# Kernel optimization log

Measured on AMD Instinct MI355X. Metric: run time of the kernel, lower is better.

The kernel has to match this reference:

```python
import jax, jax.numpy as jnp
import numpy as np


def _gcn_conv(x, src, dst, W, b, num_nodes, deg_inv_sqrt):
    # PyG GCNConv: h = x @ W, then normalized scatter-add over edges (incl. self loops), + bias
    h = x @ W  # [N, d_out]
    norm = deg_inv_sqrt[src] * deg_inv_sqrt[dst]  # [E']
    msg = h[src] * norm[:, None]  # gather + scale, [E', d_out]
    out = jax.ops.segment_sum(msg, dst, num_segments=num_nodes)  # scatter-add to targets
    return out + b


def reference(x, edge_index, W1, b1, W2, b2, num_nodes):
    src0, dst0 = edge_index[0], edge_index[1]
    loop = jnp.arange(num_nodes, dtype=edge_index.dtype)
    # add self loops (PyG default add_self_loops=True)
    src = jnp.concatenate([src0, loop])
    dst = jnp.concatenate([dst0, loop])
    # symmetric normalization D^{-1/2} (A+I) D^{-1/2}, degree from self-looped graph
    deg = jax.ops.segment_sum(jnp.ones_like(src, dtype=x.dtype), dst, num_segments=num_nodes)
    deg_inv_sqrt = jnp.where(deg > 0, jax.lax.rsqrt(jnp.maximum(deg, 1)), 0.0).astype(x.dtype)

    z = jax.nn.relu(_gcn_conv(x, src, dst, W1, b1, num_nodes, deg_inv_sqrt))
    z = jax.nn.relu(_gcn_conv(z, src, dst, W2, b2, num_nodes, deg_inv_sqrt))
    return z


def setup_inputs() -> dict:
    key = jax.random.key(0)
    k1, k2, k3, k4 = jax.random.split(key, 4)
    N, E, D, H = 50000, 1600000, 128, 128
    x = jax.random.normal(k1, (N, D), dtype=jnp.float32)
    edge_index = jax.random.randint(k2, (2, E), 0, N, dtype=jnp.int64)
    s = 1.0 / np.sqrt(D)
    W1 = jax.random.normal(k3, (D, H), dtype=jnp.float32) * s
    W2 = jax.random.normal(k4, (H, H), dtype=jnp.float32) * s
    return {
        "x": x,
        "edge_index": edge_index,
        "W1": W1,
        "b1": jnp.zeros((H,), jnp.float32),
        "W2": W2,
        "b2": jnp.zeros((H,), jnp.float32),
        "num_nodes": N,
    }
```

## Files before the change

### kernel.cpp

```cpp
#include <hip/hip_runtime.h>

#define FD 128
#define BSH 7
#define BPAD 16
#define CH 4096
#define CHT 16

typedef __attribute__((ext_vector_type(8))) short bf16x8;
typedef __attribute__((ext_vector_type(4))) float f32x4;

__device__ inline unsigned bfr(float f) {
    unsigned u = __float_as_uint(f);
    return (u + 0x7FFF + ((u >> 16) & 1)) >> 16;
}
__device__ inline float uplo(unsigned p) { return __uint_as_float(p << 16); }
__device__ inline float uphi(unsigned p) { return __uint_as_float(p & 0xFFFF0000u); }


__global__ __launch_bounds__(256) void hist_kernel(
        const int* __restrict__ dst, int* __restrict__ bhist, int E, int K) {
    __shared__ int lh[512];
    for (int i = threadIdx.x; i < K; i += 256) lh[i] = 0;
    __syncthreads();
    for (int e = blockIdx.x * 256 + threadIdx.x; e < E; e += gridDim.x * 256)
        atomicAdd(&lh[dst[e] >> BSH], 1);
    __syncthreads();
    for (int i = threadIdx.x; i < K; i += 256)
        if (lh[i]) atomicAdd(&bhist[i], lh[i]);
}

__global__ __launch_bounds__(512) void bscan_kernel(
        const int* __restrict__ bhist, int* __restrict__ bbase, int* __restrict__ bcur,
        int* __restrict__ rp, int K, int E, int N) {
    __shared__ int sm[512];
    int t = threadIdx.x;
    int v = (t < K) ? bhist[t] : 0;
    sm[t] = v;
    __syncthreads();
    for (int off = 1; off < 512; off <<= 1) {
        int add = (t >= off) ? sm[t - off] : 0;
        __syncthreads();
        sm[t] += add;
        __syncthreads();
    }
    if (t < K) { bbase[t] = sm[t] - v; bcur[t * BPAD] = sm[t] - v; }
    if (t == 0) { bbase[K] = E; rp[N] = E; }
}

__global__ __launch_bounds__(256) void partition_kernel(
        const int* __restrict__ src, const int* __restrict__ dst,
        int* __restrict__ bcur, int* __restrict__ pairs, int E) {
    __shared__ int   lcnt[512];
    __shared__ int   lstart[512];
    __shared__ int   ldelta[512];
    __shared__ int   sm[256];
    __shared__ int   staged[CH];
    __shared__ short binof[CH];
    int t = threadIdx.x;
    int base = blockIdx.x * CH;
    int n = min(CH, E - base);

    lcnt[t] = 0; lcnt[t + 256] = 0;
    __syncthreads();

    int pk[CHT]; int bn[CHT];
    #pragma unroll
    for (int j = 0; j < CHT; ++j) {
        int i = t + j * 256;
        bn[j] = -1;
        if (i < n) {
            int d = dst[base + i];
            int s = src[base + i];
            bn[j] = d >> BSH;
            pk[j] = ((d & ((1 << BSH) - 1)) << 17) | s;
            atomicAdd(&lcnt[bn[j]], 1);
        }
    }
    __syncthreads();

    int c0 = lcnt[2 * t], c1 = lcnt[2 * t + 1];
    int s2 = c0 + c1;
    sm[t] = s2;
    __syncthreads();
    for (int off = 1; off < 256; off <<= 1) {
        int add = (t >= off) ? sm[t - off] : 0;
        __syncthreads();
        sm[t] += add;
        __syncthreads();
    }
    int ex = sm[t] - s2;
    lstart[2 * t] = ex;     lstart[2 * t + 1] = ex + c0;
    lcnt[2 * t]   = ex;     lcnt[2 * t + 1]   = ex + c0;
    __syncthreads();

    #pragma unroll
    for (int j = 0; j < CHT; ++j) {
        if (bn[j] >= 0) {
            int pos = atomicAdd(&lcnt[bn[j]], 1);
            staged[pos] = pk[j];
            binof[pos] = (short)bn[j];
        }
    }
    __syncthreads();

    #pragma unroll
    for (int k = 0; k < 2; ++k) {
        int b = 2 * t + k;
        int cnt = lcnt[b] - lstart[b];
        if (cnt > 0) {
            int g = atomicAdd(&bcur[b * BPAD], cnt);
            ldelta[b] = g - lstart[b];
        }
    }
    __syncthreads();

    for (int i = t; i < n; i += 256)
        pairs[ldelta[binof[i]] + i] = staged[i];
}

__global__ __launch_bounds__(256) void build_kernel(
        const int* __restrict__ pairs, const int* __restrict__ bbase,
        int* __restrict__ rp, float* __restrict__ dis, int* __restrict__ col, int N) {
    __shared__ int lcnt[1 << BSH];
    __shared__ int lsum[1 << BSH];
    __shared__ int lbase[1 << BSH];
    int b = blockIdx.x;
    int t = threadIdx.x;
    int nbase = b << BSH;
    int nn = min(1 << BSH, N - nbase);
    int beg = bbase[b], end = bbase[b + 1];
    if (t < 128) lcnt[t] = 0;
    __syncthreads();
    for (int e = beg + t; e < end; e += 256)
        atomicAdd(&lcnt[pairs[e] >> 17], 1);
    __syncthreads();
    if (t < 128) lsum[t] = lcnt[t];
    __syncthreads();
    for (int off = 1; off < 128; off <<= 1) {
        int add = (t < 128 && t >= off) ? lsum[t - off] : 0;
        __syncthreads();
        if (t < 128) lsum[t] += add;
        __syncthreads();
    }
    if (t < 128) {
        int excl = beg + lsum[t] - lcnt[t];
        lbase[t] = excl;
        if (t < nn) {
            rp[nbase + t] = excl;
            dis[nbase + t] = rsqrtf((float)(lcnt[t] + 1));
        }
    }
    __syncthreads();
    if (t < 128) lcnt[t] = lbase[t];
    __syncthreads();
    for (int e = beg + t; e < end; e += 256) {
        int p = pairs[e];
        int pos = atomicAdd(&lcnt[p >> 17], 1);
        col[pos] = p & 0x1FFFF;
    }
}


__global__ void cvt_kernel(const float4* __restrict__ in, uint2* __restrict__ outp, int n4) {
    int i = blockIdx.x * blockDim.x + threadIdx.x;
    if (i < n4) {
        float4 v = in[i];
        uint2 o;
        o.x = bfr(v.x) | (bfr(v.y) << 16);
        o.y = bfr(v.z) | (bfr(v.w) << 16);
        outp[i] = o;
    }
}

__global__ void wt_kernel(const float* __restrict__ W, unsigned short* __restrict__ WT) {
    int k = blockIdx.x;
    int n = threadIdx.x;
    WT[n * FD + k] = (unsigned short)bfr(W[k * FD + n]);
}


#define APAD 8
#define ASTR (FD + APAD)

__global__ __launch_bounds__(256) void gemm_mfma(
        const unsigned short* __restrict__ A, const unsigned short* __restrict__ WT,
        const float* __restrict__ dis, unsigned short* __restrict__ C, int M) {
    __shared__ unsigned short As[128 * ASTR];
    __shared__ unsigned short Bs[128 * ASTR];
    int tid = threadIdx.x;
    int lane = tid & 63;
    int wave = tid >> 6;
    int quad = lane >> 4;
    int l16 = lane & 15;
    int rowBase = blockIdx.x * 128;

    #pragma unroll
    for (int p = 0; p < 8; ++p) {
        int r = p * 16 + (tid >> 4);
        int cq = (tid & 15) * 8;
        uint4 v = make_uint4(0u, 0u, 0u, 0u);
        int gr = rowBase + r;
        if (gr < M) v = *(const uint4*)&A[(size_t)gr * FD + cq];
        *(uint4*)&As[r * ASTR + cq] = v;
        *(uint4*)&Bs[r * ASTR + cq] = *(const uint4*)&WT[(size_t)r * FD + cq];
    }
    __syncthreads();

    int m0 = wave * 32;
    f32x4 acc[2][8] = {};
    #pragma unroll
    for (int kt = 0; kt < 4; ++kt) {
        int ko = kt * 32 + quad * 8;
        bf16x8 a0 = *(bf16x8*)&As[(m0 + l16) * ASTR + ko];
        bf16x8 a1 = *(bf16x8*)&As[(m0 + 16 + l16) * ASTR + ko];
        #pragma unroll
        for (int n = 0; n < 8; ++n) {
            bf16x8 b = *(bf16x8*)&Bs[(n * 16 + l16) * ASTR + ko];
            acc[0][n] = __builtin_amdgcn_mfma_f32_16x16x32_bf16(a0, b, acc[0][n], 0, 0, 0);
            acc[1][n] = __builtin_amdgcn_mfma_f32_16x16x32_bf16(a1, b, acc[1][n], 0, 0, 0);
        }
    }

    #pragma unroll
    for (int ms = 0; ms < 2; ++ms) {
        #pragma unroll
        for (int r = 0; r < 4; ++r) {
            int grow = rowBase + m0 + ms * 16 + quad * 4 + r;
            if (grow < M) {
                float dv = dis[grow];
                #pragma unroll
                for (int n = 0; n < 8; ++n) {
                    C[(size_t)grow * FD + n * 16 + l16] =
                        (unsigned short)bfr(dv * acc[ms][n][r]);
                }
            }
        }
    }
}


__global__ __launch_bounds__(256) void agg_kernel(
        const unsigned* __restrict__ h, const float* __restrict__ dis,
        const int* __restrict__ rp, const int* __restrict__ col,
        const float2* __restrict__ bias, void* __restrict__ out, int N, int obf) {
    int v = blockIdx.x * 4 + threadIdx.y;
    v = __builtin_amdgcn_readfirstlane(v);
    if (v >= N) return;
    int t = threadIdx.x;
    float dv = dis[v];
    size_t vb = (size_t)v * 64 + t;
    unsigned hp = h[vb];
    float2 acc;
    acc.x = uplo(hp); acc.y = uphi(hp);
    int e = rp[v];
    int end = rp[v + 1];
    for (; e + 8 <= end; e += 8) {
        int u0 = col[e],     u1 = col[e + 1], u2 = col[e + 2], u3 = col[e + 3];
        int u4 = col[e + 4], u5 = col[e + 5], u6 = col[e + 6], u7 = col[e + 7];
        unsigned p0 = h[(size_t)u0 * 64 + t];
        unsigned p1 = h[(size_t)u1 * 64 + t];
        unsigned p2 = h[(size_t)u2 * 64 + t];
        unsigned p3 = h[(size_t)u3 * 64 + t];
        unsigned p4 = h[(size_t)u4 * 64 + t];
        unsigned p5 = h[(size_t)u5 * 64 + t];
        unsigned p6 = h[(size_t)u6 * 64 + t];
        unsigned p7 = h[(size_t)u7 * 64 + t];
        acc.x += uplo(p0); acc.y += uphi(p0);
        acc.x += uplo(p1); acc.y += uphi(p1);
        acc.x += uplo(p2); acc.y += uphi(p2);
        acc.x += uplo(p3); acc.y += uphi(p3);
        acc.x += uplo(p4); acc.y += uphi(p4);
        acc.x += uplo(p5); acc.y += uphi(p5);
        acc.x += uplo(p6); acc.y += uphi(p6);
        acc.x += uplo(p7); acc.y += uphi(p7);
    }
    for (; e < end; ++e) {
        unsigned p = h[(size_t)col[e] * 64 + t];
        acc.x += uplo(p); acc.y += uphi(p);
    }
    float2 bb = bias[t];
    float2 r;
    r.x = fmaxf(fmaf(dv, acc.x, bb.x), 0.0f);
    r.y = fmaxf(fmaf(dv, acc.y, bb.y), 0.0f);
    if (obf) {
        ((unsigned*)out)[vb] = bfr(r.x) | (bfr(r.y) << 16);
    } else {
        ((float2*)out)[vb] = r;
    }
}


extern "C" void kernel_launch(void* const* d_in, const int* in_sizes, int n_in,
                              void* d_out, int out_size, void* d_ws, size_t ws_size,
                              hipStream_t stream) {
    const float* x  = (const float*)d_in[0];
    const int*   ei = (const int*)d_in[1];
    const float* W1 = (const float*)d_in[2];
    const float* b1 = (const float*)d_in[3];
    const float* W2 = (const float*)d_in[4];
    const float* b2 = (const float*)d_in[5];

    int N = in_sizes[0] / FD;
    int E = in_sizes[1] / 2;
    const int* src = ei;
    const int* dst = ei + E;
    int K = (N + (1 << BSH) - 1) >> BSH;

    char* base = (char*)d_ws;
    size_t off = 0;
    auto align256 = [](size_t v) { return (v + 255) & ~(size_t)255; };
    int*            rp    = (int*)(base + off);            off += align256((size_t)(N + 1) * 4);
    float*          dis   = (float*)(base + off);          off += align256((size_t)N * 4);
    int*            bhist = (int*)(base + off);            off += align256(512 * 4);
    int*            bbase = (int*)(base + off);            off += align256(513 * 4);
    int*            bcur  = (int*)(base + off);            off += align256((size_t)K * BPAD * 4);
    unsigned short* w1t   = (unsigned short*)(base + off); off += align256((size_t)FD * FD * 2);
    unsigned short* w2t   = (unsigned short*)(base + off); off += align256((size_t)FD * FD * 2);
    int*            col   = (int*)(base + off);            off += align256((size_t)E * 4);
    unsigned short* hbuf  = (unsigned short*)(base + off); off += align256((size_t)N * FD * 2);
    unsigned short* xz    = (unsigned short*)(base + off); off += align256((size_t)N * FD * 2);
    int*            pairs = (int*)(base + off);            off += align256((size_t)E * 4);
    (void)ws_size; (void)n_in; (void)out_size;

    int PB = (E + CH - 1) / CH;
    int n4 = N * FD / 4;

    hipMemsetAsync(bhist, 0, 512 * 4, stream);
    hist_kernel     <<<1024, 256, 0, stream>>>(dst, bhist, E, K);
    bscan_kernel    <<<1, 512, 0, stream>>>(bhist, bbase, bcur, rp, K, E, N);
    partition_kernel<<<PB, 256, 0, stream>>>(src, dst, bcur, pairs, E);
    build_kernel    <<<K, 256, 0, stream>>>(pairs, bbase, rp, dis, col, N);

    cvt_kernel<<<(n4 + 255) / 256, 256, 0, stream>>>((const float4*)x, (uint2*)xz, n4);
    wt_kernel <<<FD, FD, 0, stream>>>(W1, w1t);
    wt_kernel <<<FD, FD, 0, stream>>>(W2, w2t);

    dim3 aggBlk(64, 4);
    int aggGrid = (N + 3) / 4;
    int gemmGrid = (N + 127) / 128;

    gemm_mfma<<<gemmGrid, 256, 0, stream>>>(xz, w1t, dis, hbuf, N);
    agg_kernel<<<aggGrid, aggBlk, 0, stream>>>((const unsigned*)hbuf, dis, rp, col,
                                               (const float2*)b1, xz, N, 1);
    gemm_mfma<<<gemmGrid, 256, 0, stream>>>(xz, w2t, dis, hbuf, N);
    agg_kernel<<<aggGrid, aggBlk, 0, stream>>>((const unsigned*)hbuf, dis, rp, col,
                                               (const float2*)b2, d_out, N, 0);
}
```

Baseline: 277.7 us.

## Fuse x conversion into GEMM, merge weight transposes, split agg wave across edges

Drops the separate fp32-to-bf16 conversion kernel for x by converting inside the first GEMM's tile load, and merges the two weight-transpose launches into one. The aggregation kernel now has each half-wave handle alternate neighbor edges with 8-byte non-temporal loads, combining the halves with a cross-lane shuffle. The hist grid is also halved. This removes a full read/write pass over x and a couple of launches, and raises the number of gathers in flight per wave, at the cost of extra shuffle work and a half-idle tail.

```diff
diff --git a/kernel.cpp b/kernel.cpp
--- a/kernel.cpp
+++ b/kernel.cpp
@@ -8,6 +8,7 @@
 
 typedef __attribute__((ext_vector_type(8))) short bf16x8;
 typedef __attribute__((ext_vector_type(4))) float f32x4;
+typedef __attribute__((ext_vector_type(2))) unsigned int u32x2;
 
 __device__ inline unsigned bfr(float f) {
     unsigned u = __float_as_uint(f);
@@ -161,30 +162,23 @@
 }
 
 
-__global__ void cvt_kernel(const float4* __restrict__ in, uint2* __restrict__ outp, int n4) {
-    int i = blockIdx.x * blockDim.x + threadIdx.x;
-    if (i < n4) {
-        float4 v = in[i];
-        uint2 o;
-        o.x = bfr(v.x) | (bfr(v.y) << 16);
-        o.y = bfr(v.z) | (bfr(v.w) << 16);
-        outp[i] = o;
-    }
-}
-
-__global__ void wt_kernel(const float* __restrict__ W, unsigned short* __restrict__ WT) {
-    int k = blockIdx.x;
+__global__ void wt_kernel(const float* __restrict__ W1, unsigned short* __restrict__ W1T,
+                          const float* __restrict__ W2, unsigned short* __restrict__ W2T) {
+    int k = blockIdx.x & (FD - 1);
     int n = threadIdx.x;
-    WT[n * FD + k] = (unsigned short)bfr(W[k * FD + n]);
+    if (blockIdx.x < FD) W1T[n * FD + k] = (unsigned short)bfr(W1[k * FD + n]);
+    else                 W2T[n * FD + k] = (unsigned short)bfr(W2[k * FD + n]);
 }
 
 
 #define APAD 8
 #define ASTR (FD + APAD)
 
-__global__ __launch_bounds__(256) void gemm_mfma(
-        const unsigned short* __restrict__ A, const unsigned short* __restrict__ WT,
-        const float* __restrict__ dis, unsigned short* __restrict__ C, int M) {
+template <bool A32>
+__device__ void gemm_body(const void* __restrict__ Ap,
+                          const unsigned short* __restrict__ WT,
+                          const float* __restrict__ dis,
+                          unsigned short* __restrict__ C, int M) {
     __shared__ unsigned short As[128 * ASTR];
     __shared__ unsigned short Bs[128 * ASTR];
     int tid = threadIdx.x;
@@ -198,9 +192,21 @@
     for (int p = 0; p < 8; ++p) {
         int r = p * 16 + (tid >> 4);
         int cq = (tid & 15) * 8;
+        int gr = rowBase + r;
         uint4 v = make_uint4(0u, 0u, 0u, 0u);
-        int gr = rowBase + r;
-        if (gr < M) v = *(const uint4*)&A[(size_t)gr * FD + cq];
+        if (A32) {
+            if (gr < M) {
+                const float* a = (const float*)Ap + (size_t)gr * FD + cq;
+                float4 f0 = *(const float4*)a;
+                float4 f1 = *(const float4*)(a + 4);
+                v.x = bfr(f0.x) | (bfr(f0.y) << 16);
+                v.y = bfr(f0.z) | (bfr(f0.w) << 16);
+                v.z = bfr(f1.x) | (bfr(f1.y) << 16);
+                v.w = bfr(f1.z) | (bfr(f1.w) << 16);
+            }
+        } else {
+            if (gr < M) v = *(const uint4*)((const unsigned short*)Ap + (size_t)gr * FD + cq);
+        }
         *(uint4*)&As[r * ASTR + cq] = v;
         *(uint4*)&Bs[r * ASTR + cq] = *(const uint4*)&WT[(size_t)r * FD + cq];
     }
@@ -238,54 +244,88 @@
     }
 }
 
+__global__ __launch_bounds__(256) void gemm_mfma_f32(
+        const float* __restrict__ A, const unsigned short* __restrict__ WT,
+        const float* __restrict__ dis, unsigned short* __restrict__ C, int M) {
+    gemm_body<true>(A, WT, dis, C, M);
+}
+
+__global__ __launch_bounds__(256) void gemm_mfma_bf16(
+        const unsigned short* __restrict__ A, const unsigned short* __restrict__ WT,
+        const float* __restrict__ dis, unsigned short* __restrict__ C, int M) {
+    gemm_body<false>(A, WT, dis, C, M);
+}
+
 
 __global__ __launch_bounds__(256) void agg_kernel(
         const unsigned* __restrict__ h, const float* __restrict__ dis,
         const int* __restrict__ rp, const int* __restrict__ col,
-        const float2* __restrict__ bias, void* __restrict__ out, int N, int obf) {
+        const float4* __restrict__ bias, void* __restrict__ out, int N, int obf) {
     int v = blockIdx.x * 4 + threadIdx.y;
     v = __builtin_amdgcn_readfirstlane(v);
     if (v >= N) return;
     int t = threadIdx.x;
-    float dv = dis[v];
-    size_t vb = (size_t)v * 64 + t;
-    unsigned hp = h[vb];
-    float2 acc;
-    acc.x = uplo(hp); acc.y = uphi(hp);
+    int tl = t & 31;
+    int hh = t >> 5;
+    float4 acc = make_float4(0.f, 0.f, 0.f, 0.f);
     int e = rp[v];
     int end = rp[v + 1];
-    for (; e + 8 <= end; e += 8) {
-        int u0 = col[e],     u1 = col[e + 1], u2 = col[e + 2], u3 = col[e + 3];
-        int u4 = col[e + 4], u5 = col[e + 5], u6 = col[e + 6], u7 = col[e + 7];
-        unsigned p0 = h[(size_t)u0 * 64 + t];
-        unsigned p1 = h[(size_t)u1 * 64 + t];
-        unsigned p2 = h[(size_t)u2 * 64 + t];
-        unsigned p3 = h[(size_t)u3 * 64 + t];
-        unsigned p4 = h[(size_t)u4 * 64 + t];
-        unsigned p5 = h[(size_t)u5 * 64 + t];
-        unsigned p6 = h[(size_t)u6 * 64 + t];
-        unsigned p7 = h[(size_t)u7 * 64 + t];
-        acc.x += uplo(p0); acc.y += uphi(p0);
-        acc.x += uplo(p1); acc.y += uphi(p1);
-        acc.x += uplo(p2); acc.y += uphi(p2);
-        acc.x += uplo(p3); acc.y += uphi(p3);
-        acc.x += uplo(p4); acc.y += uphi(p4);
-        acc.x += uplo(p5); acc.y += uphi(p5);
-        acc.x += uplo(p6); acc.y += uphi(p6);
-        acc.x += uplo(p7); acc.y += uphi(p7);
-    }
-    for (; e < end; ++e) {
-        unsigned p = h[(size_t)col[e] * 64 + t];
-        acc.x += uplo(p); acc.y += uphi(p);
-    }
-    float2 bb = bias[t];
-    float2 r;
-    r.x = fmaxf(fmaf(dv, acc.x, bb.x), 0.0f);
-    r.y = fmaxf(fmaf(dv, acc.y, bb.y), 0.0f);
-    if (obf) {
-        ((unsigned*)out)[vb] = bfr(r.x) | (bfr(r.y) << 16);
-    } else {
-        ((float2*)out)[vb] = r;
+
+    for (; e + 16 <= end; e += 16) {
+        int u[8];
+        #pragma unroll
+        for (int j = 0; j < 8; ++j) {
+            int a = col[e + 2 * j];
+            int b = col[e + 2 * j + 1];
+            u[j] = hh ? b : a;
+        }
+        #pragma unroll
+        for (int j = 0; j < 8; ++j) {
+            u32x2 p = __builtin_nontemporal_load((const u32x2*)(h + (size_t)u[j] * 64) + tl);
+            acc.x += uplo(p.x); acc.y += uphi(p.x);
+            acc.z += uplo(p.y); acc.w += uphi(p.y);
+        }
+    }
+    for (; e + 2 <= end; e += 2) {
+        int a = col[e], b = col[e + 1];
+        int uu = hh ? b : a;
+        u32x2 p = __builtin_nontemporal_load((const u32x2*)(h + (size_t)uu * 64) + tl);
+        acc.x += uplo(p.x); acc.y += uphi(p.x);
+        acc.z += uplo(p.y); acc.w += uphi(p.y);
+    }
+    if (e < end) {
+        int a = col[e];
+        u32x2 p = __builtin_nontemporal_load((const u32x2*)(h + (size_t)a * 64) + tl);
+        if (hh == 0) {
+            acc.x += uplo(p.x); acc.y += uphi(p.x);
+            acc.z += uplo(p.y); acc.w += uphi(p.y);
+        }
+    }
+
+    acc.x += __shfl_xor(acc.x, 32);
+    acc.y += __shfl_xor(acc.y, 32);
+    acc.z += __shfl_xor(acc.z, 32);
+    acc.w += __shfl_xor(acc.w, 32);
+
+    if (hh == 0) {
+        u32x2 p = *((const u32x2*)(h + (size_t)v * 64) + tl);
+        acc.x += uplo(p.x); acc.y += uphi(p.x);
+        acc.z += uplo(p.y); acc.w += uphi(p.y);
+        float dv = dis[v];
+        float4 bb = bias[tl];
+        float4 r;
+        r.x = fmaxf(fmaf(dv, acc.x, bb.x), 0.0f);
+        r.y = fmaxf(fmaf(dv, acc.y, bb.y), 0.0f);
+        r.z = fmaxf(fmaf(dv, acc.z, bb.z), 0.0f);
+        r.w = fmaxf(fmaf(dv, acc.w, bb.w), 0.0f);
+        if (obf) {
+            uint2 o;
+            o.x = bfr(r.x) | (bfr(r.y) << 16);
+            o.y = bfr(r.z) | (bfr(r.w) << 16);
+            ((uint2*)out)[(size_t)v * 32 + tl] = o;
+        } else {
+            ((float4*)out)[(size_t)v * 32 + tl] = r;
+        }
     }
 }
 
@@ -318,31 +358,28 @@
     unsigned short* w2t   = (unsigned short*)(base + off); off += align256((size_t)FD * FD * 2);
     int*            col   = (int*)(base + off);            off += align256((size_t)E * 4);
     unsigned short* hbuf  = (unsigned short*)(base + off); off += align256((size_t)N * FD * 2);
-    unsigned short* xz    = (unsigned short*)(base + off); off += align256((size_t)N * FD * 2);
+    unsigned short* z1    = (unsigned short*)(base + off); off += align256((size_t)N * FD * 2);
     int*            pairs = (int*)(base + off);            off += align256((size_t)E * 4);
     (void)ws_size; (void)n_in; (void)out_size;
 
     int PB = (E + CH - 1) / CH;
-    int n4 = N * FD / 4;
-
-    hipMemsetAsync(bhist, 0, 512 * 4, stream);
-    hist_kernel     <<<1024, 256, 0, stream>>>(dst, bhist, E, K);
+
+    (void)hipMemsetAsync(bhist, 0, 512 * 4, stream);
+    hist_kernel     <<<512, 256, 0, stream>>>(dst, bhist, E, K);
     bscan_kernel    <<<1, 512, 0, stream>>>(bhist, bbase, bcur, rp, K, E, N);
     partition_kernel<<<PB, 256, 0, stream>>>(src, dst, bcur, pairs, E);
     build_kernel    <<<K, 256, 0, stream>>>(pairs, bbase, rp, dis, col, N);
 
-    cvt_kernel<<<(n4 + 255) / 256, 256, 0, stream>>>((const float4*)x, (uint2*)xz, n4);
-    wt_kernel <<<FD, FD, 0, stream>>>(W1, w1t);
-    wt_kernel <<<FD, FD, 0, stream>>>(W2, w2t);
+    wt_kernel<<<2 * FD, FD, 0, stream>>>(W1, w1t, W2, w2t);
 
     dim3 aggBlk(64, 4);
     int aggGrid = (N + 3) / 4;
     int gemmGrid = (N + 127) / 128;
 
-    gemm_mfma<<<gemmGrid, 256, 0, stream>>>(xz, w1t, dis, hbuf, N);
+    gemm_mfma_f32 <<<gemmGrid, 256, 0, stream>>>(x, w1t, dis, hbuf, N);
     agg_kernel<<<aggGrid, aggBlk, 0, stream>>>((const unsigned*)hbuf, dis, rp, col,
-                                               (const float2*)b1, xz, N, 1);
-    gemm_mfma<<<gemmGrid, 256, 0, stream>>>(xz, w2t, dis, hbuf, N);
+                                               (const float4*)b1, z1, N, 1);
+    gemm_mfma_bf16<<<gemmGrid, 256, 0, stream>>>(z1, w2t, dis, hbuf, N);
     agg_kernel<<<aggGrid, aggBlk, 0, stream>>>((const unsigned*)hbuf, dis, rp, col,
-                                               (const float2*)b2, d_out, N, 0);
-}
+                                               (const float4*)b2, d_out, N, 0);
+}
```

Measured after the change: 311.7 us. +12.3%, slower.
